# Kernel tuning notes

Measured on AMD Instinct MI355X. Metric: run time of the kernel, lower is better.

Reference implementation:

```python
import jax, jax.numpy as jnp
import numpy as np

V, F, N = 5143, 10144, 2_000_000


def _safe_normalize(x):
    # matches GaussianAvatars safe_normalize: x / sqrt(clamp(|x|^2, min=1e-20))
    return x * jax.lax.rsqrt(jnp.clip(jnp.sum(x * x, axis=-1, keepdims=True), 1e-20, None))


def _quat_wxyz_to_rotmat(q):
    # rotation_activation (L2 normalize with eps) then wxyz->xyzw + roma unitquat_to_rotmat
    q = q / (jnp.sqrt(jnp.sum(q * q, axis=-1, keepdims=True)) + 1e-12)
    w, x, y, z = q[..., 0], q[..., 1], q[..., 2], q[..., 3]
    R = jnp.stack([
        jnp.stack([1 - 2 * (y * y + z * z), 2 * (x * y - z * w), 2 * (x * z + y * w)], axis=-1),
        jnp.stack([2 * (x * y + z * w), 1 - 2 * (x * x + z * z), 2 * (y * z - x * w)], axis=-1),
        jnp.stack([2 * (x * z - y * w), 2 * (y * z + x * w), 1 - 2 * (x * x + y * y)], axis=-1),
    ], axis=-2)
    return R  # [N,3,3]


def setup_inputs() -> dict:
    key = jax.random.key(0)
    ks = jax.random.split(key, 9)
    verts = jax.random.normal(ks[0], (V, 3), jnp.float32) * 0.1
    faces = jax.random.randint(ks[1], (F, 3), 0, V, dtype=jnp.int32)
    binding = jax.random.randint(ks[2], (N,), 0, F, dtype=jnp.int32)
    xyz = jax.random.normal(ks[3], (N, 3), jnp.float32) * 0.01
    rotation = jax.random.normal(ks[4], (N, 4), jnp.float32)
    scaling = jax.random.normal(ks[5], (N, 3), jnp.float32) - 4.0
    opacity = jax.random.normal(ks[6], (N, 1), jnp.float32)
    features_dc = jax.random.normal(ks[7], (N, 1, 3), jnp.float32)
    features_rest = jax.random.normal(ks[8], (N, 15, 3), jnp.float32) * 0.1
    return dict(verts=verts, faces=faces, binding=binding, xyz=xyz, rotation=rotation,
                scaling=scaling, opacity=opacity, features_dc=features_dc,
                features_rest=features_rest)


def reference(verts, faces, binding, xyz, rotation, scaling, opacity, features_dc, features_rest):
    # --- per-face geometry (compute_face_orientation + face_center) ---
    v0 = verts[faces[:, 0]]  # [F,3]
    v1 = verts[faces[:, 1]]
    v2 = verts[faces[:, 2]]
    face_center = (v0 + v1 + v2) / 3.0  # triangles.mean(dim=-2)
    e01 = v1 - v0
    e02 = v2 - v0
    a0 = _safe_normalize(e01)
    a1 = _safe_normalize(jnp.cross(a0, e02))
    a2 = -_safe_normalize(jnp.cross(a1, a0))
    face_orien_mat = jnp.stack([a0, a1, a2], axis=-1)  # [F,3,3], columns = axes
    s0 = jnp.sqrt(jnp.sum(e01 * e01, axis=-1, keepdims=True))
    s1 = jnp.abs(jnp.sum(a2 * e02, axis=-1, keepdims=True))
    face_scaling = 0.5 * (s0 + s1)  # [F,1]

    # --- binding-indexed gathers ---
    O_b = face_orien_mat[binding]      # [N,3,3]
    fs_b = face_scaling[binding]       # [N,1]
    fc_b = face_center[binding]        # [N,3]

    # --- gaussian position in world space ---
    xyz_out = jnp.einsum('nij,nj->ni', O_b, xyz) * fs_b + fc_b  # [N,3]

    # --- color (dc sh band 0 + opacity), scaled to 0..255 ---
    op = jax.nn.sigmoid(opacity)  # [N,1]
    color = jnp.clip((jnp.concatenate([0.5 + 0.282 * features_dc[:, 0, :], op], axis=-1)) * 255.0, 0.0, 255.0)

    # --- covariance build ---
    scales = jnp.exp(scaling) * fs_b  # [N,3]
    Q = _quat_wxyz_to_rotmat(rotation)  # [N,3,3]
    rotations = jnp.swapaxes(jnp.einsum('nij,njk->nik', O_b, Q), 1, 2)  # (O@Q)^T, [N,3,3]
    sig = rotations * scales[:, :, None]  # einsum('bij,bi->bij')
    C = jnp.einsum('nij,nik->njk', sig, sig)  # [N,3,3] = sig^T sig
    simga = jnp.stack([C[:, 0, 0], C[:, 0, 1], C[:, 0, 2], C[:, 1, 1], C[:, 1, 2], C[:, 2, 2]], axis=-1)

    return jnp.concatenate([xyz_out, color, simga], axis=-1)  # [N,13]
```

## Files before the change

kernel.cpp:

```cpp
#include <hip/hip_runtime.h>
#include <math.h>

struct F3 { float x, y, z; };

__device__ __forceinline__ F3 f3(float x, float y, float z) { return {x, y, z}; }
__device__ __forceinline__ F3 add(F3 a, F3 b) { return {a.x+b.x, a.y+b.y, a.z+b.z}; }
__device__ __forceinline__ F3 sub(F3 a, F3 b) { return {a.x-b.x, a.y-b.y, a.z-b.z}; }
__device__ __forceinline__ F3 mul(F3 a, float s) { return {a.x*s, a.y*s, a.z*s}; }
__device__ __forceinline__ float dot3(F3 a, F3 b) { return a.x*b.x + a.y*b.y + a.z*b.z; }
__device__ __forceinline__ F3 cross3(F3 a, F3 b) {
    return {a.y*b.z - a.z*b.y, a.z*b.x - a.x*b.z, a.x*b.y - a.y*b.x};
}
__device__ __forceinline__ F3 safe_normalize(F3 a) {
    float d = dot3(a, a);
    float inv = rsqrtf(fmaxf(d, 1e-20f));
    return mul(a, inv);
}

#define BLK 256

__global__ __launch_bounds__(BLK) void face_precompute_kernel(
    const float* __restrict__ verts, const int* __restrict__ faces,
    float4* __restrict__ tab, int F)
{
    const int f = blockIdx.x * BLK + threadIdx.x;
    if (f >= F) return;
    const int f0 = faces[3*f+0], f1 = faces[3*f+1], f2 = faces[3*f+2];
    const F3 v0 = f3(verts[3*f0], verts[3*f0+1], verts[3*f0+2]);
    const F3 v1 = f3(verts[3*f1], verts[3*f1+1], verts[3*f1+2]);
    const F3 v2 = f3(verts[3*f2], verts[3*f2+1], verts[3*f2+2]);

    const F3 fc  = mul(add(add(v0, v1), v2), (1.0f/3.0f));
    const F3 e01 = sub(v1, v0);
    const F3 e02 = sub(v2, v0);
    const F3 a0 = safe_normalize(e01);
    const F3 a1 = safe_normalize(cross3(a0, e02));
    const F3 a2 = mul(safe_normalize(cross3(a1, a0)), -1.0f);
    const float s0 = sqrtf(dot3(e01, e01));
    const float s1 = fabsf(dot3(a2, e02));
    const float fs = 0.5f * (s0 + s1);

    tab[4*f+0] = make_float4(fc.x, fc.y, fc.z, fs);
    tab[4*f+1] = make_float4(a0.x, a0.y, a0.z, 0.0f);
    tab[4*f+2] = make_float4(a1.x, a1.y, a1.z, 0.0f);
}

struct Out13 {
    float x0, x1, x2;
    float c0, c1, c2, c3;
    float s0, s1, s2, s3, s4, s5;
};

__device__ __forceinline__ Out13 compute_point(
    float px, float py, float pz,
    float qw, float qx, float qy, float qz,
    float sc0, float sc1, float sc2,
    float opa, float d0, float d1, float d2,
    float4 t0, float4 t1, float4 t2)
{
    const F3 fc = f3(t0.x, t0.y, t0.z);
    const float fs = t0.w;
    const F3 a0 = f3(t1.x, t1.y, t1.z);
    const F3 a1 = f3(t2.x, t2.y, t2.z);
    const F3 a2 = cross3(a0, a1);

    F3 xo = add(add(mul(a0, px), mul(a1, py)), mul(a2, pz));
    xo = add(mul(xo, fs), fc);

    const float qn = sqrtf(qw*qw + qx*qx + qy*qy + qz*qz) + 1e-12f;
    const float qinv = 1.0f / qn;
    const float w = qw*qinv, x = qx*qinv, y = qy*qinv, z = qz*qinv;
    const float Q00 = 1.0f - 2.0f*(y*y + z*z);
    const float Q01 = 2.0f*(x*y - z*w);
    const float Q02 = 2.0f*(x*z + y*w);
    const float Q10 = 2.0f*(x*y + z*w);
    const float Q11 = 1.0f - 2.0f*(x*x + z*z);
    const float Q12 = 2.0f*(y*z - x*w);
    const float Q20 = 2.0f*(x*z - y*w);
    const float Q21 = 2.0f*(y*z + x*w);
    const float Q22 = 1.0f - 2.0f*(x*x + y*y);

    const F3 m0 = add(add(mul(a0, Q00), mul(a1, Q10)), mul(a2, Q20));
    const F3 m1 = add(add(mul(a0, Q01), mul(a1, Q11)), mul(a2, Q21));
    const F3 m2 = add(add(mul(a0, Q02), mul(a1, Q12)), mul(a2, Q22));

    const float w0 = __expf(sc0) * fs;
    const float w1 = __expf(sc1) * fs;
    const float w2 = __expf(sc2) * fs;
    const float t0s = w0*w0, t1s = w1*w1, t2s = w2*w2;

    Out13 o;
    o.s0 = t0s*m0.x*m0.x + t1s*m1.x*m1.x + t2s*m2.x*m2.x;
    o.s1 = t0s*m0.x*m0.y + t1s*m1.x*m1.y + t2s*m2.x*m2.y;
    o.s2 = t0s*m0.x*m0.z + t1s*m1.x*m1.z + t2s*m2.x*m2.z;
    o.s3 = t0s*m0.y*m0.y + t1s*m1.y*m1.y + t2s*m2.y*m2.y;
    o.s4 = t0s*m0.y*m0.z + t1s*m1.y*m1.z + t2s*m2.y*m2.z;
    o.s5 = t0s*m0.z*m0.z + t1s*m1.z*m1.z + t2s*m2.z*m2.z;

    const float sg = 1.0f / (1.0f + __expf(-opa));
    o.x0 = xo.x; o.x1 = xo.y; o.x2 = xo.z;
    o.c0 = fminf(fmaxf((0.5f + 0.282f*d0) * 255.0f, 0.0f), 255.0f);
    o.c1 = fminf(fmaxf((0.5f + 0.282f*d1) * 255.0f, 0.0f), 255.0f);
    o.c2 = fminf(fmaxf((0.5f + 0.282f*d2) * 255.0f, 0.0f), 255.0f);
    o.c3 = fminf(fmaxf(sg * 255.0f, 0.0f), 255.0f);
    return o;
}

__global__ __launch_bounds__(BLK) void gauss_main_kernel(
    const float4* __restrict__ tab,
    const int*    __restrict__ binding,
    const float*  __restrict__ xyz,
    const float*  __restrict__ rot,
    const float*  __restrict__ scal,
    const float*  __restrict__ opac,
    const float*  __restrict__ fdc,
    float*        __restrict__ out,
    int N)
{
    __shared__ float sin_[3 * BLK * 3];
    __shared__ float sout[BLK * 13];

    const int tid  = threadIdx.x;
    const int base = blockIdx.x * BLK;
    const int i    = base + tid;
    const int count = min(BLK, N - base);
    const bool full = (count == BLK);

    const int b = (i < N) ? binding[i] : 0;

    if (full) {
        const float4* x4 = reinterpret_cast<const float4*>(xyz  + (size_t)base * 3);
        const float4* s4 = reinterpret_cast<const float4*>(scal + (size_t)base * 3);
        const float4* f4 = reinterpret_cast<const float4*>(fdc  + (size_t)base * 3);
        float4* sv = reinterpret_cast<float4*>(sin_);
        if (tid < 192) {
            sv[      tid] = x4[tid];
            sv[192 + tid] = s4[tid];
            sv[384 + tid] = f4[tid];
        }
    }

    float4 q4 = make_float4(0,0,0,1);
    float opa = 0.0f;
    float4 t0 = make_float4(0,0,0,0), t1 = t0, t2 = t0;
    if (i < N) {
        q4  = reinterpret_cast<const float4*>(rot)[i];
        opa = opac[i];
        t0  = tab[4*b+0];
        t1  = tab[4*b+1];
        t2  = tab[4*b+2];
    }

    float px, py, pz, sc0, sc1, sc2, d0, d1, d2;
    if (full) {
        __syncthreads();
        px  = sin_[        3*tid    ]; py  = sin_[        3*tid + 1]; pz  = sin_[        3*tid + 2];
        sc0 = sin_[ 768 +  3*tid    ]; sc1 = sin_[ 768 +  3*tid + 1]; sc2 = sin_[ 768 +  3*tid + 2];
        d0  = sin_[1536 +  3*tid    ]; d1  = sin_[1536 +  3*tid + 1]; d2  = sin_[1536 +  3*tid + 2];
    } else {
        px = py = pz = sc0 = sc1 = sc2 = d0 = d1 = d2 = 0.0f;
        if (i < N) {
            px  = xyz [3*i]; py  = xyz [3*i+1]; pz  = xyz [3*i+2];
            sc0 = scal[3*i]; sc1 = scal[3*i+1]; sc2 = scal[3*i+2];
            d0  = fdc [3*i]; d1  = fdc [3*i+1]; d2  = fdc [3*i+2];
        }
    }

    if (i < N) {
        const Out13 o = compute_point(px, py, pz,
                                      q4.x, q4.y, q4.z, q4.w,
                                      sc0, sc1, sc2, opa, d0, d1, d2,
                                      t0, t1, t2);
        float* s = sout + tid * 13;
        s[0] = o.x0; s[1] = o.x1; s[2]  = o.x2;
        s[3] = o.c0; s[4] = o.c1; s[5]  = o.c2; s[6] = o.c3;
        s[7] = o.s0; s[8] = o.s1; s[9]  = o.s2;
        s[10] = o.s3; s[11] = o.s4; s[12] = o.s5;
    }

    __syncthreads();

    const int total = count * 13;
    const size_t obase = (size_t)base * 13;
    const int n4 = total >> 2;
    const float4* sf = reinterpret_cast<const float4*>(sout);
    float4* o4 = reinterpret_cast<float4*>(out + obase);
    for (int j = tid; j < n4; j += BLK) o4[j] = sf[j];
    for (int j = (n4 << 2) + tid; j < total; j += BLK) out[obase + j] = sout[j];
}

__global__ __launch_bounds__(BLK) void gauss_fused_kernel(
    const float* __restrict__ verts, const int* __restrict__ faces,
    const int* __restrict__ binding, const float* __restrict__ xyz,
    const float* __restrict__ rot, const float* __restrict__ scal,
    const float* __restrict__ opac, const float* __restrict__ fdc,
    float* __restrict__ out, int N)
{
    const int i = blockIdx.x * BLK + threadIdx.x;
    if (i >= N) return;
    const int b = binding[i];
    const int f0 = faces[3*b+0], f1 = faces[3*b+1], f2 = faces[3*b+2];
    const F3 v0 = f3(verts[3*f0], verts[3*f0+1], verts[3*f0+2]);
    const F3 v1 = f3(verts[3*f1], verts[3*f1+1], verts[3*f1+2]);
    const F3 v2 = f3(verts[3*f2], verts[3*f2+1], verts[3*f2+2]);
    const F3 fc  = mul(add(add(v0, v1), v2), (1.0f/3.0f));
    const F3 e01 = sub(v1, v0);
    const F3 e02 = sub(v2, v0);
    const F3 a0 = safe_normalize(e01);
    const F3 a1 = safe_normalize(cross3(a0, e02));
    const float s0 = sqrtf(dot3(e01, e01));
    const F3 a2r = mul(safe_normalize(cross3(a1, a0)), -1.0f);
    const float s1 = fabsf(dot3(a2r, e02));
    const float fs = 0.5f * (s0 + s1);

    const Out13 o = compute_point(xyz[3*i], xyz[3*i+1], xyz[3*i+2],
                                  rot[4*i], rot[4*i+1], rot[4*i+2], rot[4*i+3],
                                  scal[3*i], scal[3*i+1], scal[3*i+2],
                                  opac[i], fdc[3*i], fdc[3*i+1], fdc[3*i+2],
                                  make_float4(fc.x, fc.y, fc.z, fs),
                                  make_float4(a0.x, a0.y, a0.z, 0.0f),
                                  make_float4(a1.x, a1.y, a1.z, 0.0f));
    float* op = out + (size_t)i * 13;
    op[0] = o.x0; op[1] = o.x1; op[2]  = o.x2;
    op[3] = o.c0; op[4] = o.c1; op[5]  = o.c2; op[6] = o.c3;
    op[7] = o.s0; op[8] = o.s1; op[9]  = o.s2;
    op[10] = o.s3; op[11] = o.s4; op[12] = o.s5;
}

extern "C" void kernel_launch(void* const* d_in, const int* in_sizes, int n_in,
                              void* d_out, int out_size, void* d_ws, size_t ws_size,
                              hipStream_t stream) {
    const float* verts   = (const float*)d_in[0];
    const int*   faces   = (const int*)  d_in[1];
    const int*   binding = (const int*)  d_in[2];
    const float* xyz     = (const float*)d_in[3];
    const float* rot     = (const float*)d_in[4];
    const float* scal    = (const float*)d_in[5];
    const float* opac    = (const float*)d_in[6];
    const float* fdc     = (const float*)d_in[7];
    float* out = (float*)d_out;
    const int N = in_sizes[2];
    const int F = in_sizes[1] / 3;

    const size_t tab_bytes = (size_t)F * 4 * sizeof(float4);
    const int blocks = (N + BLK - 1) / BLK;

    if (ws_size >= tab_bytes) {
        float4* tab = (float4*)d_ws;
        const int fblocks = (F + BLK - 1) / BLK;
        face_precompute_kernel<<<fblocks, BLK, 0, stream>>>(verts, faces, tab, F);
        gauss_main_kernel<<<blocks, BLK, 0, stream>>>(
            tab, binding, xyz, rot, scal, opac, fdc, out, N);
    } else {
        gauss_fused_kernel<<<blocks, BLK, 0, stream>>>(
            verts, faces, binding, xyz, rot, scal, opac, fdc, out, N);
    }
}
```

Measured before the change: 45.69 us.

## Store face frame as quaternion, compose quaternions, use nontemporal loads and stores

The face precompute now turns each face's orientation matrix into a unit quaternion and writes a 2-float4 record per face instead of a 3-float4 one. The main kernel rotates the position with the quaternion and multiplies the face and gaussian quaternions before building the rotation matrix, which shrinks the gathered table. Streaming inputs and the output are read and written with nontemporal builtins to keep them out of the cache. The matrix-to-quaternion conversion branches and adds arithmetic per point, and it may differ slightly in rounding from the matrix path.

```diff
diff --git a/kernel.cpp b/kernel.cpp
--- a/kernel.cpp
+++ b/kernel.cpp
@@ -1,5 +1,7 @@
 #include <hip/hip_runtime.h>
 #include <math.h>
+
+typedef float f4 __attribute__((ext_vector_type(4)));
 
 struct F3 { float x, y, z; };
 
@@ -21,7 +23,7 @@
 
 __global__ __launch_bounds__(BLK) void face_precompute_kernel(
     const float* __restrict__ verts, const int* __restrict__ faces,
-    float4* __restrict__ tab, int F)
+    f4* __restrict__ tab, int F)
 {
     const int f = blockIdx.x * BLK + threadIdx.x;
     if (f >= F) return;
@@ -40,81 +42,54 @@
     const float s1 = fabsf(dot3(a2, e02));
     const float fs = 0.5f * (s0 + s1);
 
-    tab[4*f+0] = make_float4(fc.x, fc.y, fc.z, fs);
-    tab[4*f+1] = make_float4(a0.x, a0.y, a0.z, 0.0f);
-    tab[4*f+2] = make_float4(a1.x, a1.y, a1.z, 0.0f);
-}
-
-struct Out13 {
-    float x0, x1, x2;
-    float c0, c1, c2, c3;
-    float s0, s1, s2, s3, s4, s5;
-};
-
-__device__ __forceinline__ Out13 compute_point(
-    float px, float py, float pz,
-    float qw, float qx, float qy, float qz,
-    float sc0, float sc1, float sc2,
-    float opa, float d0, float d1, float d2,
-    float4 t0, float4 t1, float4 t2)
-{
-    const F3 fc = f3(t0.x, t0.y, t0.z);
-    const float fs = t0.w;
-    const F3 a0 = f3(t1.x, t1.y, t1.z);
-    const F3 a1 = f3(t2.x, t2.y, t2.z);
-    const F3 a2 = cross3(a0, a1);
-
-    F3 xo = add(add(mul(a0, px), mul(a1, py)), mul(a2, pz));
-    xo = add(mul(xo, fs), fc);
-
-    const float qn = sqrtf(qw*qw + qx*qx + qy*qy + qz*qz) + 1e-12f;
-    const float qinv = 1.0f / qn;
-    const float w = qw*qinv, x = qx*qinv, y = qy*qinv, z = qz*qinv;
-    const float Q00 = 1.0f - 2.0f*(y*y + z*z);
-    const float Q01 = 2.0f*(x*y - z*w);
-    const float Q02 = 2.0f*(x*z + y*w);
-    const float Q10 = 2.0f*(x*y + z*w);
-    const float Q11 = 1.0f - 2.0f*(x*x + z*z);
-    const float Q12 = 2.0f*(y*z - x*w);
-    const float Q20 = 2.0f*(x*z - y*w);
-    const float Q21 = 2.0f*(y*z + x*w);
-    const float Q22 = 1.0f - 2.0f*(x*x + y*y);
-
-    const F3 m0 = add(add(mul(a0, Q00), mul(a1, Q10)), mul(a2, Q20));
-    const F3 m1 = add(add(mul(a0, Q01), mul(a1, Q11)), mul(a2, Q21));
-    const F3 m2 = add(add(mul(a0, Q02), mul(a1, Q12)), mul(a2, Q22));
-
-    const float w0 = __expf(sc0) * fs;
-    const float w1 = __expf(sc1) * fs;
-    const float w2 = __expf(sc2) * fs;
-    const float t0s = w0*w0, t1s = w1*w1, t2s = w2*w2;
-
-    Out13 o;
-    o.s0 = t0s*m0.x*m0.x + t1s*m1.x*m1.x + t2s*m2.x*m2.x;
-    o.s1 = t0s*m0.x*m0.y + t1s*m1.x*m1.y + t2s*m2.x*m2.y;
-    o.s2 = t0s*m0.x*m0.z + t1s*m1.x*m1.z + t2s*m2.x*m2.z;
-    o.s3 = t0s*m0.y*m0.y + t1s*m1.y*m1.y + t2s*m2.y*m2.y;
-    o.s4 = t0s*m0.y*m0.z + t1s*m1.y*m1.z + t2s*m2.y*m2.z;
-    o.s5 = t0s*m0.z*m0.z + t1s*m1.z*m1.z + t2s*m2.z*m2.z;
-
-    const float sg = 1.0f / (1.0f + __expf(-opa));
-    o.x0 = xo.x; o.x1 = xo.y; o.x2 = xo.z;
-    o.c0 = fminf(fmaxf((0.5f + 0.282f*d0) * 255.0f, 0.0f), 255.0f);
-    o.c1 = fminf(fmaxf((0.5f + 0.282f*d1) * 255.0f, 0.0f), 255.0f);
-    o.c2 = fminf(fmaxf((0.5f + 0.282f*d2) * 255.0f, 0.0f), 255.0f);
-    o.c3 = fminf(fmaxf(sg * 255.0f, 0.0f), 255.0f);
-    return o;
+    const float R00 = a0.x, R10 = a0.y, R20 = a0.z;
+    const float R01 = a1.x, R11 = a1.y, R21 = a1.z;
+    const float R02 = a2.x, R12 = a2.y, R22 = a2.z;
+    float qw, qx, qy, qz;
+    const float tr = R00 + R11 + R22;
+    if (tr > 0.0f) {
+        const float s = 0.5f / sqrtf(tr + 1.0f);
+        qw = 0.25f / s;
+        qx = (R21 - R12) * s;
+        qy = (R02 - R20) * s;
+        qz = (R10 - R01) * s;
+    } else if (R00 > R11 && R00 > R22) {
+        const float s = 2.0f * sqrtf(1.0f + R00 - R11 - R22);
+        qw = (R21 - R12) / s;
+        qx = 0.25f * s;
+        qy = (R01 + R10) / s;
+        qz = (R02 + R20) / s;
+    } else if (R11 > R22) {
+        const float s = 2.0f * sqrtf(1.0f + R11 - R00 - R22);
+        qw = (R02 - R20) / s;
+        qx = (R01 + R10) / s;
+        qy = 0.25f * s;
+        qz = (R12 + R21) / s;
+    } else {
+        const float s = 2.0f * sqrtf(1.0f + R22 - R00 - R11);
+        qw = (R10 - R01) / s;
+        qx = (R02 + R20) / s;
+        qy = (R12 + R21) / s;
+        qz = 0.25f * s;
+    }
+    const float qn = rsqrtf(fmaxf(qw*qw + qx*qx + qy*qy + qz*qz, 1e-30f));
+    qw *= qn; qx *= qn; qy *= qn; qz *= qn;
+
+    f4 r0; r0.x = fc.x; r0.y = fc.y; r0.z = fc.z; r0.w = fs;
+    f4 r1; r1.x = qw;   r1.y = qx;   r1.z = qy;   r1.w = qz;
+    tab[2*f+0] = r0;
+    tab[2*f+1] = r1;
 }
 
 __global__ __launch_bounds__(BLK) void gauss_main_kernel(
-    const float4* __restrict__ tab,
-    const int*    __restrict__ binding,
-    const float*  __restrict__ xyz,
-    const float*  __restrict__ rot,
-    const float*  __restrict__ scal,
-    const float*  __restrict__ opac,
-    const float*  __restrict__ fdc,
-    float*        __restrict__ out,
+    const f4*    __restrict__ tab,
+    const int*   __restrict__ binding,
+    const float* __restrict__ xyz,
+    const float* __restrict__ rot,
+    const float* __restrict__ scal,
+    const float* __restrict__ opac,
+    const float* __restrict__ fdc,
+    float*       __restrict__ out,
     int N)
 {
     __shared__ float sin_[3 * BLK * 3];
@@ -126,29 +101,28 @@
     const int count = min(BLK, N - base);
     const bool full = (count == BLK);
 
-    const int b = (i < N) ? binding[i] : 0;
+    const int b = (i < N) ? __builtin_nontemporal_load(binding + i) : 0;
+
+    f4 t0 = {0,0,0,0}, t1 = {0,0,0,1};
+    f4 q4 = {0,0,0,1};
+    float opa = 0.0f;
+    if (i < N) {
+        t0 = tab[2*b+0];
+        t1 = tab[2*b+1];
+        q4 = __builtin_nontemporal_load(reinterpret_cast<const f4*>(rot) + i);
+        opa = __builtin_nontemporal_load(opac + i);
+    }
 
     if (full) {
-        const float4* x4 = reinterpret_cast<const float4*>(xyz  + (size_t)base * 3);
-        const float4* s4 = reinterpret_cast<const float4*>(scal + (size_t)base * 3);
-        const float4* f4 = reinterpret_cast<const float4*>(fdc  + (size_t)base * 3);
-        float4* sv = reinterpret_cast<float4*>(sin_);
+        const f4* x4 = reinterpret_cast<const f4*>(xyz  + (size_t)base * 3);
+        const f4* s4 = reinterpret_cast<const f4*>(scal + (size_t)base * 3);
+        const f4* d4 = reinterpret_cast<const f4*>(fdc  + (size_t)base * 3);
+        f4* sv = reinterpret_cast<f4*>(sin_);
         if (tid < 192) {
-            sv[      tid] = x4[tid];
-            sv[192 + tid] = s4[tid];
-            sv[384 + tid] = f4[tid];
+            sv[      tid] = __builtin_nontemporal_load(x4 + tid);
+            sv[192 + tid] = __builtin_nontemporal_load(s4 + tid);
+            sv[384 + tid] = __builtin_nontemporal_load(d4 + tid);
         }
-    }
-
-    float4 q4 = make_float4(0,0,0,1);
-    float opa = 0.0f;
-    float4 t0 = make_float4(0,0,0,0), t1 = t0, t2 = t0;
-    if (i < N) {
-        q4  = reinterpret_cast<const float4*>(rot)[i];
-        opa = opac[i];
-        t0  = tab[4*b+0];
-        t1  = tab[4*b+1];
-        t2  = tab[4*b+2];
     }
 
     float px, py, pz, sc0, sc1, sc2, d0, d1, d2;
@@ -167,15 +141,56 @@
     }
 
     if (i < N) {
-        const Out13 o = compute_point(px, py, pz,
-                                      q4.x, q4.y, q4.z, q4.w,
-                                      sc0, sc1, sc2, opa, d0, d1, d2,
-                                      t0, t1, t2);
+        const F3 fc = f3(t0.x, t0.y, t0.z);
+        const float fs = t0.w;
+        const float fw = t1.x, fx = t1.y, fy = t1.z, fz = t1.w;
+
+        const F3 p = f3(px, py, pz);
+        const F3 qv = f3(fx, fy, fz);
+        const F3 tt = mul(cross3(qv, p), 2.0f);
+        const F3 v  = add(add(p, mul(tt, fw)), cross3(qv, tt));
+        const F3 xo = add(mul(v, fs), fc);
+
+        const float qn = sqrtf(q4.x*q4.x + q4.y*q4.y + q4.z*q4.z + q4.w*q4.w) + 1e-12f;
+        const float qi = 1.0f / qn;
+        const float pw = q4.x*qi, pxq = q4.y*qi, pyq = q4.z*qi, pzq = q4.w*qi;
+
+        const float tw = fw*pw  - fx*pxq - fy*pyq - fz*pzq;
+        const float tx = fw*pxq + fx*pw  + fy*pzq - fz*pyq;
+        const float ty = fw*pyq - fx*pzq + fy*pw  + fz*pxq;
+        const float tz = fw*pzq + fx*pyq - fy*pxq + fz*pw;
+
+        const F3 m0 = f3(1.0f - 2.0f*(ty*ty + tz*tz),
+                         2.0f*(tx*ty + tz*tw),
+                         2.0f*(tx*tz - ty*tw));
+        const F3 m1 = f3(2.0f*(tx*ty - tz*tw),
+                         1.0f - 2.0f*(tx*tx + tz*tz),
+                         2.0f*(ty*tz + tx*tw));
+        const F3 m2 = f3(2.0f*(tx*tz + ty*tw),
+                         2.0f*(ty*tz - tx*tw),
+                         1.0f - 2.0f*(tx*tx + ty*ty));
+
+        const float w0 = __expf(sc0) * fs;
+        const float w1 = __expf(sc1) * fs;
+        const float w2 = __expf(sc2) * fs;
+        const float t0s = w0*w0, t1s = w1*w1, t2s = w2*w2;
+
+        const float C00 = t0s*m0.x*m0.x + t1s*m1.x*m1.x + t2s*m2.x*m2.x;
+        const float C01 = t0s*m0.x*m0.y + t1s*m1.x*m1.y + t2s*m2.x*m2.y;
+        const float C02 = t0s*m0.x*m0.z + t1s*m1.x*m1.z + t2s*m2.x*m2.z;
+        const float C11 = t0s*m0.y*m0.y + t1s*m1.y*m1.y + t2s*m2.y*m2.y;
+        const float C12 = t0s*m0.y*m0.z + t1s*m1.y*m1.z + t2s*m2.y*m2.z;
+        const float C22 = t0s*m0.z*m0.z + t1s*m1.z*m1.z + t2s*m2.z*m2.z;
+
+        const float sg = 1.0f / (1.0f + __expf(-opa));
+
         float* s = sout + tid * 13;
-        s[0] = o.x0; s[1] = o.x1; s[2]  = o.x2;
-        s[3] = o.c0; s[4] = o.c1; s[5]  = o.c2; s[6] = o.c3;
-        s[7] = o.s0; s[8] = o.s1; s[9]  = o.s2;
-        s[10] = o.s3; s[11] = o.s4; s[12] = o.s5;
+        s[0]  = xo.x; s[1] = xo.y; s[2] = xo.z;
+        s[3]  = fminf(fmaxf((0.5f + 0.282f*d0) * 255.0f, 0.0f), 255.0f);
+        s[4]  = fminf(fmaxf((0.5f + 0.282f*d1) * 255.0f, 0.0f), 255.0f);
+        s[5]  = fminf(fmaxf((0.5f + 0.282f*d2) * 255.0f, 0.0f), 255.0f);
+        s[6]  = fminf(fmaxf(sg * 255.0f, 0.0f), 255.0f);
+        s[7]  = C00; s[8] = C01; s[9] = C02; s[10] = C11; s[11] = C12; s[12] = C22;
     }
 
     __syncthreads();
@@ -183,9 +198,9 @@
     const int total = count * 13;
     const size_t obase = (size_t)base * 13;
     const int n4 = total >> 2;
-    const float4* sf = reinterpret_cast<const float4*>(sout);
-    float4* o4 = reinterpret_cast<float4*>(out + obase);
-    for (int j = tid; j < n4; j += BLK) o4[j] = sf[j];
+    const f4* sf = reinterpret_cast<const f4*>(sout);
+    f4* o4 = reinterpret_cast<f4*>(out + obase);
+    for (int j = tid; j < n4; j += BLK) __builtin_nontemporal_store(sf[j], o4 + j);
     for (int j = (n4 << 2) + tid; j < total; j += BLK) out[obase + j] = sout[j];
 }
 
@@ -209,22 +224,53 @@
     const F3 a0 = safe_normalize(e01);
     const F3 a1 = safe_normalize(cross3(a0, e02));
     const float s0 = sqrtf(dot3(e01, e01));
-    const F3 a2r = mul(safe_normalize(cross3(a1, a0)), -1.0f);
-    const float s1 = fabsf(dot3(a2r, e02));
+    const F3 a2 = mul(safe_normalize(cross3(a1, a0)), -1.0f);
+    const float s1 = fabsf(dot3(a2, e02));
     const float fs = 0.5f * (s0 + s1);
 
-    const Out13 o = compute_point(xyz[3*i], xyz[3*i+1], xyz[3*i+2],
-                                  rot[4*i], rot[4*i+1], rot[4*i+2], rot[4*i+3],
-                                  scal[3*i], scal[3*i+1], scal[3*i+2],
-                                  opac[i], fdc[3*i], fdc[3*i+1], fdc[3*i+2],
-                                  make_float4(fc.x, fc.y, fc.z, fs),
-                                  make_float4(a0.x, a0.y, a0.z, 0.0f),
-                                  make_float4(a1.x, a1.y, a1.z, 0.0f));
+    const float px = xyz[3*i], py = xyz[3*i+1], pz = xyz[3*i+2];
+    const float qw0 = rot[4*i], qx0 = rot[4*i+1], qy0 = rot[4*i+2], qz0 = rot[4*i+3];
+    const float sc0 = scal[3*i], sc1 = scal[3*i+1], sc2 = scal[3*i+2];
+    const float opa = opac[i];
+    const float d0 = fdc[3*i], d1 = fdc[3*i+1], d2 = fdc[3*i+2];
+
+    F3 xo = add(add(mul(a0, px), mul(a1, py)), mul(a2, pz));
+    xo = add(mul(xo, fs), fc);
+
+    const float qn = sqrtf(qw0*qw0 + qx0*qx0 + qy0*qy0 + qz0*qz0) + 1e-12f;
+    const float qi = 1.0f / qn;
+    const float w = qw0*qi, x = qx0*qi, y = qy0*qi, z = qz0*qi;
+    const float Q00 = 1.0f - 2.0f*(y*y + z*z);
+    const float Q01 = 2.0f*(x*y - z*w);
+    const float Q02 = 2.0f*(x*z + y*w);
+    const float Q10 = 2.0f*(x*y + z*w);
+    const float Q11 = 1.0f - 2.0f*(x*x + z*z);
+    const float Q12 = 2.0f*(y*z - x*w);
+    const float Q20 = 2.0f*(x*z - y*w);
+    const float Q21 = 2.0f*(y*z + x*w);
+    const float Q22 = 1.0f - 2.0f*(x*x + y*y);
+
+    const F3 m0 = add(add(mul(a0, Q00), mul(a1, Q10)), mul(a2, Q20));
+    const F3 m1 = add(add(mul(a0, Q01), mul(a1, Q11)), mul(a2, Q21));
+    const F3 m2 = add(add(mul(a0, Q02), mul(a1, Q12)), mul(a2, Q22));
+
+    const float w0 = __expf(sc0) * fs;
+    const float w1 = __expf(sc1) * fs;
+    const float w2 = __expf(sc2) * fs;
+    const float t0s = w0*w0, t1s = w1*w1, t2s = w2*w2;
+
     float* op = out + (size_t)i * 13;
-    op[0] = o.x0; op[1] = o.x1; op[2]  = o.x2;
-    op[3] = o.c0; op[4] = o.c1; op[5]  = o.c2; op[6] = o.c3;
-    op[7] = o.s0; op[8] = o.s1; op[9]  = o.s2;
-    op[10] = o.s3; op[11] = o.s4; op[12] = o.s5;
+    op[0] = xo.x; op[1] = xo.y; op[2] = xo.z;
+    op[3] = fminf(fmaxf((0.5f + 0.282f*d0) * 255.0f, 0.0f), 255.0f);
+    op[4] = fminf(fmaxf((0.5f + 0.282f*d1) * 255.0f, 0.0f), 255.0f);
+    op[5] = fminf(fmaxf((0.5f + 0.282f*d2) * 255.0f, 0.0f), 255.0f);
+    op[6] = fminf(fmaxf((1.0f/(1.0f+__expf(-opa))) * 255.0f, 0.0f), 255.0f);
+    op[7]  = t0s*m0.x*m0.x + t1s*m1.x*m1.x + t2s*m2.x*m2.x;
+    op[8]  = t0s*m0.x*m0.y + t1s*m1.x*m1.y + t2s*m2.x*m2.y;
+    op[9]  = t0s*m0.x*m0.z + t1s*m1.x*m1.z + t2s*m2.x*m2.z;
+    op[10] = t0s*m0.y*m0.y + t1s*m1.y*m1.y + t2s*m2.y*m2.y;
+    op[11] = t0s*m0.y*m0.z + t1s*m1.y*m1.z + t2s*m2.y*m2.z;
+    op[12] = t0s*m0.z*m0.z + t1s*m1.z*m1.z + t2s*m2.z*m2.z;
 }
 
 extern "C" void kernel_launch(void* const* d_in, const int* in_sizes, int n_in,
@@ -242,11 +288,11 @@
     const int N = in_sizes[2];
     const int F = in_sizes[1] / 3;
 
-    const size_t tab_bytes = (size_t)F * 4 * sizeof(float4);
+    const size_t tab_bytes = (size_t)F * 2 * sizeof(f4);
     const int blocks = (N + BLK - 1) / BLK;
 
     if (ws_size >= tab_bytes) {
-        float4* tab = (float4*)d_ws;
+        f4* tab = (f4*)d_ws;
         const int fblocks = (F + BLK - 1) / BLK;
         face_precompute_kernel<<<fblocks, BLK, 0, stream>>>(verts, faces, tab, F);
         gauss_main_kernel<<<blocks, BLK, 0, stream>>>(
```

Result: slower. 55.28 us (+21.0%).
